# Kernel optimization log

Hardware: AMD Instinct MI355X
Metric: run time of the kernel (lower is better)

Reference implementation:

```python
import jax, jax.numpy as jnp
import numpy as np

VOCAB, D, H = 32000, 1024, 16
DH = D // H
DFF = 4 * D
EPS = 1e-5


def layer_norm(x, g, b):
    mu = jnp.mean(x, axis=-1, keepdims=True)
    var = jnp.var(x, axis=-1, keepdims=True)
    return (x - mu) * jax.lax.rsqrt(var + EPS) * g + b


def pos_enc(seq_len, d_model):
    # faithful to the torch double-loop: angle = pos / 10000**(2*i/d) for even index i
    pos = jnp.arange(seq_len, dtype=jnp.float32)[:, None]          # [S,1]
    i_even = jnp.arange(0, d_model, 2, dtype=jnp.float32)[None, :]  # [1,D/2]
    angle = pos / jnp.power(10000.0, 2.0 * i_even / d_model)        # [S,D/2]
    pe = jnp.zeros((seq_len, d_model), dtype=jnp.float32)
    pe = pe.at[:, 0::2].set(jnp.sin(angle))
    pe = pe.at[:, 1::2].set(jnp.cos(angle))
    return pe


def setup_inputs() -> dict:
    key = jax.random.key(0)
    ks = jax.random.split(key, 16)
    s = 0.02
    return {
        "tokens": jax.random.randint(ks[0], (4, 2048), 0, VOCAB),
        "emb": jax.random.normal(ks[1], (VOCAB, D), jnp.float32) * s,
        "in_proj_w": jax.random.normal(ks[2], (3 * D, D), jnp.float32) * s,
        "in_proj_b": jnp.zeros((3 * D,), jnp.float32),
        "out_proj_w": jax.random.normal(ks[3], (D, D), jnp.float32) * s,
        "out_proj_b": jnp.zeros((D,), jnp.float32),
        "w1": jax.random.normal(ks[4], (DFF, D), jnp.float32) * s,
        "b1": jnp.zeros((DFF,), jnp.float32),
        "w2": jax.random.normal(ks[5], (D, DFF), jnp.float32) * s,
        "b2": jnp.zeros((D,), jnp.float32),
        "g1": jnp.ones((D,), jnp.float32),
        "beta1": jnp.zeros((D,), jnp.float32),
        "g2": jnp.ones((D,), jnp.float32),
        "beta2": jnp.zeros((D,), jnp.float32),
    }


def reference(tokens, emb, in_proj_w, in_proj_b, out_proj_w, out_proj_b,
              w1, b1, w2, b2, g1, beta1, g2, beta2):
    B, S = tokens.shape
    x = emb[tokens] + pos_enc(S, D)[None, :, :]                 # [B,S,D]
    # multi-head self-attention (eval mode, no dropout)
    qkv = x @ in_proj_w.T + in_proj_b                           # [B,S,3D]
    q, k, v = jnp.split(qkv, 3, axis=-1)
    q = q.reshape(B, S, H, DH)
    k = k.reshape(B, S, H, DH)
    v = v.reshape(B, S, H, DH)
    scores = jnp.einsum("bqhd,bkhd->bhqk", q, k) / jnp.sqrt(jnp.float32(DH))
    attn = jax.nn.softmax(scores, axis=-1)
    ctx = jnp.einsum("bhqk,bkhd->bqhd", attn, v).reshape(B, S, D)
    attn_out = ctx @ out_proj_w.T + out_proj_b
    h = layer_norm(x + attn_out, g1, beta1)
    ff = jax.nn.relu(h @ w1.T + b1) @ w2.T + b2
    return layer_norm(h + ff, g2, beta2)
```

## Files before the change

kernel.cpp:

```cpp
#include <hip/hip_runtime.h>
#include <math.h>

#define DMODEL 1024
#define NH 16
#define DHEAD 64
#define DFF 4096
#define BATCH 4
#define SEQ 2048
#define MROWS (BATCH * SEQ)
#define LNEPS 1e-5f
#define NT (SEQ / 64)

typedef __attribute__((ext_vector_type(8))) short bf16x8;
typedef __attribute__((ext_vector_type(4))) float f32x4;
typedef __attribute__((ext_vector_type(16))) float f32x16;
typedef __attribute__((ext_vector_type(4))) unsigned int u32x4;

__device__ inline unsigned short f2bf(float f) {
  unsigned int u = __float_as_uint(f);
  unsigned int r = (u + 0x7fffu + ((u >> 16) & 1u)) >> 16;
  return (unsigned short)r;
}

__device__ inline void gload16(const unsigned short* g, char* l) {
  __builtin_amdgcn_global_load_lds(
      (const __attribute__((address_space(1))) unsigned int*)g,
      (__attribute__((address_space(3))) unsigned int*)l, 16, 0, 0);
}

__device__ inline float fexp2(float x) {
  float r;
  asm("v_exp_f32 %0, %1" : "=v"(r) : "v"(x));
  return r;
}
__device__ inline unsigned int cvtpk(float lo, float hi) {
  unsigned int r;
  asm("v_cvt_pk_bf16_f32 %0, %1, %2" : "=v"(r) : "v"(lo), "v"(hi));
  return r;
}
__device__ inline void plswap(unsigned int& a, unsigned int& b) {
  asm("v_permlane32_swap_b32 %0, %1" : "+v"(a), "+v"(b));
}

__global__ __launch_bounds__(256)
void embed_kernel(const int* __restrict__ tokens, const float* __restrict__ emb,
                  float* __restrict__ X, unsigned short* __restrict__ Xb) {
  const int HALF = DMODEL / 2;
  int idx = blockIdx.x * 256 + threadIdx.x;
  if (idx >= MROWS * HALF) return;
  int row = idx / HALF;
  int j = idx - row * HALF;
  int s = row & (SEQ - 1);
  int tok = tokens[row];
  float2 e = ((const float2*)(emb + (size_t)tok * DMODEL))[j];
  float denom = powf(10000.0f, (2.0f * (float)(2 * j)) / (float)DMODEL);
  float ang = (float)s / denom;
  float sn, cs;
  sincosf(ang, &sn, &cs);
  float2 o;
  o.x = e.x + sn;
  o.y = e.y + cs;
  ((float2*)(X + (size_t)row * DMODEL))[j] = o;
  ushort2 ob;
  ob.x = f2bf(o.x); ob.y = f2bf(o.y);
  ((ushort2*)(Xb + (size_t)row * DMODEL))[j] = ob;
}

__global__ __launch_bounds__(256)
void cvt4_kernel(const float* __restrict__ a, const float* __restrict__ b,
                 const float* __restrict__ c, const float* __restrict__ d,
                 unsigned short* __restrict__ oa, unsigned short* __restrict__ ob,
                 unsigned short* __restrict__ oc, unsigned short* __restrict__ od) {
  int i = blockIdx.x * 256 + threadIdx.x;
  const float* src; unsigned short* dst; int off;
  if (i < 786432)       { src = a; dst = oa; off = 0; }
  else if (i < 1048576) { src = b; dst = ob; off = 786432; }
  else if (i < 2097152) { src = c; dst = oc; off = 1048576; }
  else                  { src = d; dst = od; off = 2097152; }
  int j = i - off;
  float4 v = ((const float4*)src)[j];
  ushort4 o;
  o.x = f2bf(v.x); o.y = f2bf(v.y); o.z = f2bf(v.z); o.w = f2bf(v.w);
  ((ushort4*)dst)[j] = o;
}

#define AOFF(buf) ((buf) * 49152)
#define BOFF(buf) ((buf) * 49152 + 32768)

__device__ inline void stageA(const unsigned short* Ag, char* smem, int buf,
                              int m0, int K, int kt, int wv, int lane) {
  int rl = lane >> 3, c = (lane & 7) ^ rl;
#pragma unroll
  for (int i = 0; i < 4; ++i) {
    int r0 = (wv * 4 + i) * 8;
    gload16(Ag + (size_t)(m0 + r0 + rl) * K + kt * 64 + c * 8,
            smem + AOFF(buf) + r0 * 128 + lane * 16);
  }
}
__device__ inline void stageB2(const unsigned short* Bg, char* smem, int buf,
                               int n0, int K, int kt, int wv, int lane) {
  int rl = lane >> 3, c = (lane & 7) ^ rl;
#pragma unroll
  for (int i = 0; i < 2; ++i) {
    int r0 = (wv * 2 + i) * 8;
    gload16(Bg + (size_t)(n0 + r0 + rl) * K + kt * 64 + c * 8,
            smem + BOFF(buf) + r0 * 128 + lane * 16);
  }
}

#define VM6 asm volatile("s_waitcnt vmcnt(6)" ::: "memory")
#define VM0 asm volatile("s_waitcnt vmcnt(0)" ::: "memory")

#define DO_PHASE(buf, mb, LOADB, STAGE_STMT, WAIT_STMT)                         \
  {                                                                             \
    bf16x8 af[2][2];                                                            \
    _Pragma("unroll") for (int mm = 0; mm < 2; ++mm) {                          \
      int arow = wm * 64 + ((mb) + mm) * 16 + fr;                               \
      _Pragma("unroll") for (int ks = 0; ks < 2; ++ks) {                        \
        int slot = (ks * 4 + fq) ^ (arow & 7);                                  \
        af[mm][ks] = *(const bf16x8*)(smem + AOFF(buf) + arow * 128 + slot * 16); \
      }                                                                         \
    }                                                                           \
    if (LOADB) {                                                                \
      _Pragma("unroll") for (int n = 0; n < 4; ++n) {                           \
        int brow = wn * 64 + n * 16 + fr;                                       \
        _Pragma("unroll") for (int ks = 0; ks < 2; ++ks) {                      \
          int slot = (ks * 4 + fq) ^ (brow & 7);                                \
          bfr[n][ks] = *(const bf16x8*)(smem + BOFF(buf) + brow * 128 + slot * 16); \
        }                                                                       \
      }                                                                         \
    }                                                                           \
    STAGE_STMT;                                                                 \
    __builtin_amdgcn_sched_barrier(0);                                          \
    __builtin_amdgcn_s_barrier();                                               \
    __builtin_amdgcn_sched_barrier(0);                                          \
    __builtin_amdgcn_s_setprio(1);                                              \
    _Pragma("unroll") for (int mm = 0; mm < 2; ++mm)                            \
      _Pragma("unroll") for (int n = 0; n < 4; ++n)                             \
        _Pragma("unroll") for (int ks = 0; ks < 2; ++ks)                        \
          acc[(mb) + mm][n] = __builtin_amdgcn_mfma_f32_16x16x32_bf16(          \
              af[mm][ks], bfr[n][ks], acc[(mb) + mm][n], 0, 0, 0);              \
    __builtin_amdgcn_s_setprio(0);                                              \
    WAIT_STMT;                                                                  \
    __builtin_amdgcn_sched_barrier(0);                                          \
    __builtin_amdgcn_s_barrier();                                               \
    __builtin_amdgcn_sched_barrier(0);                                          \
  }

__global__ __launch_bounds__(512, 2)
void gemm8(const unsigned short* __restrict__ A, const unsigned short* __restrict__ B,
           const float* __restrict__ bias, const float* __restrict__ resid,
           float* __restrict__ Cf, unsigned short* __restrict__ Cb,
           int M, int N, int K, int relu) {
  extern __shared__ char smem[];

  const int t = threadIdx.x;
  const int lane = t & 63;
  const int wv = t >> 6;
  const int wm = wv >> 1;
  const int wn = wv & 1;
  const int fr = lane & 15;
  const int fq = lane >> 4;

  const int nwg = gridDim.x;
  const int orig = blockIdx.x;
  const int q8 = nwg >> 3;
  const int wgid = (orig & 7) * q8 + (orig >> 3);
  const int stid = wgid >> 4, within = wgid & 15;
  const int sm = within & 3, sn = within >> 2;
  const int Msup = M >> 10;
  const int stm = stid % Msup, stn = stid / Msup;
  const int m0 = (stm * 4 + sm) * 256;
  const int n0 = (stn * 4 + sn) * 128;

  f32x4 acc[4][4];
#pragma unroll
  for (int m = 0; m < 4; ++m)
#pragma unroll
    for (int n = 0; n < 4; ++n) acc[m][n] = (f32x4){0.f, 0.f, 0.f, 0.f};

  const int nk = K / 64;
  const int nj = nk / 2;

  stageB2(B, smem, 0, n0, K, 0, wv, lane);
  stageA (A, smem, 0, m0, K, 0, wv, lane);
  stageB2(B, smem, 1, n0, K, 1, wv, lane);
  stageA (A, smem, 1, m0, K, 1, wv, lane);
  VM6;
  __builtin_amdgcn_sched_barrier(0);
  __builtin_amdgcn_s_barrier();
  __builtin_amdgcn_sched_barrier(0);

  for (int j = 0; j < nj - 1; ++j) {
    const int k0 = 2 * j, k1 = 2 * j + 1;
    const int s0k = k0 + 2, s1k = k1 + 2;
    const int b0 = k0 % 3, b1 = k1 % 3;
    const int sb0 = s0k % 3, sb1 = s1k % 3;
    bf16x8 bfr[4][2];
    DO_PHASE(b0, 0, true,  stageB2(B, smem, sb0, n0, K, s0k, wv, lane), );
    DO_PHASE(b0, 2, false, stageA (A, smem, sb0, m0, K, s0k, wv, lane), VM6);
    DO_PHASE(b1, 0, true,  stageB2(B, smem, sb1, n0, K, s1k, wv, lane), );
    DO_PHASE(b1, 2, false, stageA (A, smem, sb1, m0, K, s1k, wv, lane), VM6);
  }
  {
    const int b0 = (nk - 2) % 3, b1 = (nk - 1) % 3;
    bf16x8 bfr[4][2];
    DO_PHASE(b0, 0, true,  , );
    DO_PHASE(b0, 2, false, , VM0);
    DO_PHASE(b1, 0, true,  , );
    DO_PHASE(b1, 2, false, , );
  }

  float* slab = (float*)(smem + wv * 4352);
#pragma unroll
  for (int m = 0; m < 4; ++m) {
#pragma unroll
    for (int n = 0; n < 4; ++n)
#pragma unroll
      for (int j = 0; j < 4; ++j)
        slab[(fq * 4 + j) * 68 + n * 16 + fr] = acc[m][n][j];
    int rg0 = m0 + wm * 64 + m * 16;
#pragma unroll
    for (int it = 0; it < 4; ++it) {
      int u = it * 64 + lane;
      int row = u >> 4, seg = u & 15;
      float4 v = *(const float4*)&slab[row * 68 + seg * 4];
      int col = n0 + wn * 64 + seg * 4;
      float4 b4 = *(const float4*)&bias[col];
      v.x += b4.x; v.y += b4.y; v.z += b4.z; v.w += b4.w;
      if (relu) {
        v.x = fmaxf(v.x, 0.f); v.y = fmaxf(v.y, 0.f);
        v.z = fmaxf(v.z, 0.f); v.w = fmaxf(v.w, 0.f);
      }
      size_t idx = (size_t)(rg0 + row) * N + col;
      if (resid) {
        float4 r4 = *(const float4*)&resid[idx];
        v.x += r4.x; v.y += r4.y; v.z += r4.z; v.w += r4.w;
      }
      if (Cf) {
        *(float4*)&Cf[idx] = v;
      } else {
        ushort4 ob;
        ob.x = f2bf(v.x); ob.y = f2bf(v.y); ob.z = f2bf(v.z); ob.w = f2bf(v.w);
        *(ushort4*)&Cb[idx] = ob;
      }
    }
  }
}

__global__ __launch_bounds__(512, 4)
void attn_kernel(const unsigned short* __restrict__ qkv, unsigned short* __restrict__ ctxb) {
  __shared__ __align__(16) unsigned short Ks[2][64][64];
  __shared__ __align__(16) unsigned short Vts[2][64][64];
  __shared__ __align__(16) unsigned short Slab[8][32][64];

  const int t = threadIdx.x;
  const int lane = t & 63;
  const int wq = t >> 6;
  const int l31 = lane & 31;
  const int hi1 = lane >> 5;
  const int bid = blockIdx.x;
  const int bh = bid & 63;
  const int qt = bid >> 6;
  const int b = bh >> 4, h = bh & 15;
  const int q0 = qt * 256;

  const size_t RS = 3 * DMODEL;
  const unsigned short* qb = qkv + (size_t)b * SEQ * RS + h * DHEAD;
  const unsigned short* kb = qb + DMODEL;
  const unsigned short* vb = qb + 2 * DMODEL;

  bf16x8 qf[4];
  {
    const unsigned short* qrow = qb + (size_t)(q0 + wq * 32 + l31) * RS;
#pragma unroll
    for (int s = 0; s < 4; ++s)
      qf[s] = *(const bf16x8*)(qrow + s * 16 + hi1 * 8);
  }

  const unsigned short* kgl =
      kb + (size_t)(wq * 8 + (lane >> 3)) * RS + ((lane & 7) ^ (lane >> 3)) * 8;
  const int vrow0 = wq * 8;

  f32x16 oacc[2] = {};
  float lacc = 0.f;

  gload16(kgl, (char*)&Ks[0][wq * 8][0]);
  {
    unsigned int vg[8];
#pragma unroll
    for (int e = 0; e < 8; ++e)
      vg[e] = vb[(size_t)(vrow0 + e) * RS + lane];
    uint4 u;
    u.x = vg[0] | (vg[1] << 16);
    u.y = vg[2] | (vg[3] << 16);
    u.z = vg[4] | (vg[5] << 16);
    u.w = vg[6] | (vg[7] << 16);
    *(uint4*)&Vts[0][lane][((wq ^ (lane & 7)) * 8)] = u;
  }
  __syncthreads();

  const float C = 0.18033688011112042f;

  for (int kt = 0; kt < NT; ++kt) {
    const int cur = kt & 1;
    const bool more = (kt + 1 < NT);
    unsigned int vg[8];
    if (more) {
      size_t off = (size_t)(kt + 1) * 64 * RS;
      gload16(kgl + off, (char*)&Ks[cur ^ 1][wq * 8][0]);
#pragma unroll
      for (int e = 0; e < 8; ++e)
        vg[e] = vb[off + (size_t)(vrow0 + e) * RS + lane];
    }

    f32x16 sacc[2] = {};
    __builtin_amdgcn_s_setprio(1);
#pragma unroll
    for (int s = 0; s < 4; ++s) {
#pragma unroll
      for (int kvt = 0; kvt < 2; ++kvt) {
        int row = kvt * 32 + l31;
        bf16x8 kf = *(const bf16x8*)&Ks[cur][row][(((2 * s + hi1) ^ (row & 7)) * 8)];
        sacc[kvt] = __builtin_amdgcn_mfma_f32_32x32x16_bf16(kf, qf[s], sacc[kvt], 0, 0, 0);
      }
    }
    __builtin_amdgcn_s_setprio(0);

#pragma unroll
    for (int kvt = 0; kvt < 2; ++kvt) {
      float p[16];
#pragma unroll
      for (int r = 0; r < 16; ++r) p[r] = fexp2(sacc[kvt][r] * C);
      float ps = 0.f;
#pragma unroll
      for (int r = 0; r < 16; ++r) ps += p[r];
      lacc += ps;
#pragma unroll
      for (int half = 0; half < 2; ++half) {
        const int lo = half * 8;
        unsigned int x0 = cvtpk(p[lo + 0], p[lo + 1]);
        unsigned int x1 = cvtpk(p[lo + 2], p[lo + 3]);
        unsigned int y0 = cvtpk(p[lo + 4], p[lo + 5]);
        unsigned int y1 = cvtpk(p[lo + 6], p[lo + 7]);
        plswap(x0, y0);
        plswap(x1, y1);
        bf16x8 pa = __builtin_bit_cast(bf16x8, (u32x4){x0, x1, y0, y1});
        const int s2 = kvt * 2 + half;
        __builtin_amdgcn_s_setprio(1);
#pragma unroll
        for (int dt = 0; dt < 2; ++dt) {
          int vrow = dt * 32 + l31;
          bf16x8 vf = *(const bf16x8*)&Vts[cur][vrow][(((2 * s2 + hi1) ^ (vrow & 7)) * 8)];
          oacc[dt] = __builtin_amdgcn_mfma_f32_32x32x16_bf16(pa, vf, oacc[dt], 0, 0, 0);
        }
        __builtin_amdgcn_s_setprio(0);
      }
    }

    if (more) {
      uint4 u;
      u.x = vg[0] | (vg[1] << 16);
      u.y = vg[2] | (vg[3] << 16);
      u.z = vg[4] | (vg[5] << 16);
      u.w = vg[6] | (vg[7] << 16);
      *(uint4*)&Vts[cur ^ 1][lane][((wq ^ (lane & 7)) * 8)] = u;
    }
    __syncthreads();
  }

  lacc += __shfl_xor(lacc, 32);
  float inv = 1.0f / lacc;

  float iv[16];
#pragma unroll
  for (int r = 0; r < 16; ++r)
    iv[r] = __shfl(inv, (r & 3) + 8 * (r >> 2) + 4 * hi1);

#pragma unroll
  for (int dt = 0; dt < 2; ++dt) {
    const int chunk = dt * 4 + (l31 >> 3);
    const int e7 = l31 & 7;
#pragma unroll
    for (int r = 0; r < 16; ++r) {
      int qp = (r & 3) + 8 * (r >> 2) + 4 * hi1;
      Slab[wq][qp][((chunk ^ (qp & 7)) * 8) + e7] = f2bf(oacc[dt][r] * iv[r]);
    }
  }
#pragma unroll
  for (int it = 0; it < 4; ++it) {
    int u = it * 64 + lane;
    int row = u >> 3, s = u & 7;
    uint4 v = *(const uint4*)&Slab[wq][row][((s ^ (row & 7)) * 8)];
    *(uint4*)(ctxb + (size_t)(b * SEQ + q0 + wq * 32 + row) * DMODEL + h * DHEAD + s * 8) = v;
  }
}

__global__ __launch_bounds__(256)
void ln_kernel(const float* __restrict__ Z, const float* __restrict__ g,
               const float* __restrict__ bta, float* __restrict__ Y,
               unsigned short* __restrict__ Yb) {
  const int row = blockIdx.x;
  const float4* z4 = (const float4*)(Z + (size_t)row * DMODEL);
  float4 v = z4[threadIdx.x];
  float s = v.x + v.y + v.z + v.w;
  float ss = fmaf(v.x, v.x, fmaf(v.y, v.y, fmaf(v.z, v.z, v.w * v.w)));
#pragma unroll
  for (int o = 32; o >= 1; o >>= 1) {
    s += __shfl_xor(s, o);
    ss += __shfl_xor(ss, o);
  }
  __shared__ float red[8];
  int w = threadIdx.x >> 6;
  if ((threadIdx.x & 63) == 0) { red[w] = s; red[4 + w] = ss; }
  __syncthreads();
  s = red[0] + red[1] + red[2] + red[3];
  ss = red[4] + red[5] + red[6] + red[7];
  float mu = s * (1.0f / DMODEL);
  float var = ss * (1.0f / DMODEL) - mu * mu;
  float rs = rsqrtf(var + LNEPS);
  float4 gg = ((const float4*)g)[threadIdx.x];
  float4 bb = ((const float4*)bta)[threadIdx.x];
  float4 o;
  o.x = (v.x - mu) * rs * gg.x + bb.x;
  o.y = (v.y - mu) * rs * gg.y + bb.y;
  o.z = (v.z - mu) * rs * gg.z + bb.z;
  o.w = (v.w - mu) * rs * gg.w + bb.w;
  ((float4*)(Y + (size_t)row * DMODEL))[threadIdx.x] = o;
  if (Yb) {
    ushort4 ob;
    ob.x = f2bf(o.x); ob.y = f2bf(o.y); ob.z = f2bf(o.z); ob.w = f2bf(o.w);
    ((ushort4*)(Yb + (size_t)row * DMODEL))[threadIdx.x] = ob;
  }
}

extern "C" void kernel_launch(void* const* d_in, const int* in_sizes, int n_in,
                              void* d_out, int out_size, void* d_ws, size_t ws_size,
                              hipStream_t stream) {
  const int* tokens       = (const int*)d_in[0];
  const float* emb        = (const float*)d_in[1];
  const float* in_proj_w  = (const float*)d_in[2];
  const float* in_proj_b  = (const float*)d_in[3];
  const float* out_proj_w = (const float*)d_in[4];
  const float* out_proj_b = (const float*)d_in[5];
  const float* w1         = (const float*)d_in[6];
  const float* b1         = (const float*)d_in[7];
  const float* w2         = (const float*)d_in[8];
  const float* b2         = (const float*)d_in[9];
  const float* g1         = (const float*)d_in[10];
  const float* beta1      = (const float*)d_in[11];
  const float* g2         = (const float*)d_in[12];
  const float* beta2      = (const float*)d_in[13];
  float* out = (float*)d_out;

  char* ws = (char*)d_ws;
  const size_t MB = 1ull << 20;
  unsigned short* inwb  = (unsigned short*)(ws + 0 * MB);
  unsigned short* outwb = (unsigned short*)(ws + 6 * MB);
  unsigned short* w1b   = (unsigned short*)(ws + 8 * MB);
  unsigned short* w2b   = (unsigned short*)(ws + 16 * MB);
  float* x              = (float*)(ws + 24 * MB);
  unsigned short* xb    = (unsigned short*)(ws + 56 * MB);
  unsigned short* qkvb  = (unsigned short*)(ws + 72 * MB);
  unsigned short* ctxb  = (unsigned short*)(ws + 56 * MB);
  float* h              = (float*)(ws + 72 * MB);
  unsigned short* hb    = (unsigned short*)(ws + 104 * MB);
  unsigned short* ffbb  = (unsigned short*)(ws + 120 * MB);
  float* y2             = (float*)(ws + 24 * MB);

  const size_t GLDS = 147456;

  embed_kernel<<<(MROWS * (DMODEL / 2) + 255) / 256, 256, 0, stream>>>(tokens, emb, x, xb);
  cvt4_kernel<<<12288, 256, 0, stream>>>(in_proj_w, out_proj_w, w1, w2,
                                         inwb, outwb, w1b, w2b);
  gemm8<<<(MROWS / 256) * (3 * DMODEL / 128), 512, GLDS, stream>>>(
      xb, inwb, in_proj_b, nullptr, nullptr, qkvb, MROWS, 3 * DMODEL, DMODEL, 0);
  attn_kernel<<<(SEQ / 256) * (BATCH * NH), 512, 0, stream>>>(qkvb, ctxb);
  gemm8<<<(MROWS / 256) * (DMODEL / 128), 512, GLDS, stream>>>(
      ctxb, outwb, out_proj_b, x, h, nullptr, MROWS, DMODEL, DMODEL, 0);
  ln_kernel<<<MROWS, 256, 0, stream>>>(h, g1, beta1, h, hb);
  gemm8<<<(MROWS / 256) * (DFF / 128), 512, GLDS, stream>>>(
      hb, w1b, b1, nullptr, nullptr, ffbb, MROWS, DFF, DMODEL, 1);
  gemm8<<<(MROWS / 256) * (DMODEL / 128), 512, GLDS, stream>>>(
      ffbb, w2b, b2, h, y2, nullptr, MROWS, DMODEL, DFF, 0);
  ln_kernel<<<MROWS, 256, 0, stream>>>(y2, g2, beta2, out, nullptr);
}
```

Before: 411.8 us.

## Add 256x256-tile GEMM for QKV and FFN1; pre-transpose V for attention

Adds a new gemm256 kernel that uses 256x256 output tiles with double-buffered LDS and a grouped (supertile) block order, and uses it for the QKV projection and the first FFN GEMM. Larger tiles raise arithmetic intensity and cut redundant global loads. Separately, a vtrans_kernel writes V in transposed layout to the workspace, so the attention kernel can stage V with async 16-byte loads instead of scalar gathers plus an LDS repack. The cost is an extra kernel launch and extra memory traffic for the transpose. The large tiles also lower occupancy and give fewer workgroups, which can leave some CUs underused.

```diff
diff --git a/kernel.cpp b/kernel.cpp
--- a/kernel.cpp
+++ b/kernel.cpp
@@ -84,27 +84,155 @@
   ((ushort4*)dst)[j] = o;
 }
 
+__device__ inline void stage256(const unsigned short* G, char* base, int row0,
+                                int K, int kt, int t) {
+#pragma unroll
+  for (int i = 0; i < 4; ++i) {
+    int g = i * 512 + t;
+    int row = g >> 3, sl = g & 7;
+    int c = sl ^ (row & 7);
+    gload16(G + (size_t)(row0 + row) * K + kt * 64 + c * 8, base + g * 16);
+  }
+}
+
+__global__ __launch_bounds__(512, 2)
+void gemm256(const unsigned short* __restrict__ A, const unsigned short* __restrict__ B,
+             const float* __restrict__ bias, const float* __restrict__ resid,
+             float* __restrict__ Cf, unsigned short* __restrict__ Cb,
+             int M, int N, int K, int relu) {
+  extern __shared__ char smem[];
+
+  const int t = threadIdx.x;
+  const int lane = t & 63;
+  const int wv = t >> 6;
+  const int wm = wv >> 2;
+  const int wn = wv & 3;
+  const int fr = lane & 15;
+  const int fq = lane >> 4;
+
+  const int nwg = gridDim.x;
+  const int orig = blockIdx.x;
+  const int q8 = nwg >> 3;
+  const int wgid = (orig & 7) * q8 + (orig >> 3);
+  const int stid = wgid >> 2, within = wgid & 3;
+  const int sm = within & 1, sn = within >> 1;
+  const int Msup = M >> 9;
+  const int stm = stid % Msup, stn = stid / Msup;
+  const int m0 = (stm * 2 + sm) * 256;
+  const int n0 = (stn * 2 + sn) * 256;
+
+  f32x4 acc[8][4];
+#pragma unroll
+  for (int m = 0; m < 8; ++m)
+#pragma unroll
+    for (int n = 0; n < 4; ++n) acc[m][n] = (f32x4){0.f, 0.f, 0.f, 0.f};
+
+  const int nk = K / 64;
+
+  stage256(A, smem, m0, K, 0, t);
+  stage256(B, smem + 32768, n0, K, 0, t);
+
+  for (int kt = 0; kt < nk; ++kt) {
+    const int buf = kt & 1;
+    asm volatile("s_waitcnt vmcnt(0)" ::: "memory");
+    __builtin_amdgcn_s_barrier();
+    if (kt + 1 < nk) {
+      char* nxt = smem + ((buf ^ 1) << 16);
+      stage256(A, nxt, m0, K, kt + 1, t);
+      stage256(B, nxt + 32768, n0, K, kt + 1, t);
+    }
+    const unsigned short* Al = (const unsigned short*)(smem + (buf << 16));
+    const unsigned short* Bl = (const unsigned short*)(smem + (buf << 16) + 32768);
+
+    bf16x8 bfr[4][2];
+#pragma unroll
+    for (int n = 0; n < 4; ++n) {
+      int brow = wn * 64 + n * 16 + fr;
+#pragma unroll
+      for (int ks = 0; ks < 2; ++ks)
+        bfr[n][ks] = *(const bf16x8*)&Bl[brow * 64 + (((ks * 4 + fq) ^ (brow & 7)) * 8)];
+    }
+#pragma unroll
+    for (int mp = 0; mp < 4; ++mp) {
+      bf16x8 af[2][2];
+#pragma unroll
+      for (int mm = 0; mm < 2; ++mm) {
+        int arow = wm * 128 + (mp * 2 + mm) * 16 + fr;
+#pragma unroll
+        for (int ks = 0; ks < 2; ++ks)
+          af[mm][ks] = *(const bf16x8*)&Al[arow * 64 + (((ks * 4 + fq) ^ (arow & 7)) * 8)];
+      }
+      __builtin_amdgcn_s_setprio(1);
+#pragma unroll
+      for (int mm = 0; mm < 2; ++mm)
+#pragma unroll
+        for (int n = 0; n < 4; ++n)
+#pragma unroll
+          for (int ks = 0; ks < 2; ++ks)
+            acc[mp * 2 + mm][n] = __builtin_amdgcn_mfma_f32_16x16x32_bf16(
+                af[mm][ks], bfr[n][ks], acc[mp * 2 + mm][n], 0, 0, 0);
+      __builtin_amdgcn_s_setprio(0);
+    }
+  }
+
+  float* slab = (float*)(smem + wv * 4352);
+#pragma unroll
+  for (int m = 0; m < 8; ++m) {
+#pragma unroll
+    for (int n = 0; n < 4; ++n)
+#pragma unroll
+      for (int j = 0; j < 4; ++j)
+        slab[(fq * 4 + j) * 68 + n * 16 + fr] = acc[m][n][j];
+    int rg0 = m0 + wm * 128 + m * 16;
+#pragma unroll
+    for (int it = 0; it < 4; ++it) {
+      int u = it * 64 + lane;
+      int row = u >> 4, seg = u & 15;
+      float4 v = *(const float4*)&slab[row * 68 + seg * 4];
+      int col = n0 + wn * 64 + seg * 4;
+      float4 b4 = *(const float4*)&bias[col];
+      v.x += b4.x; v.y += b4.y; v.z += b4.z; v.w += b4.w;
+      if (relu) {
+        v.x = fmaxf(v.x, 0.f); v.y = fmaxf(v.y, 0.f);
+        v.z = fmaxf(v.z, 0.f); v.w = fmaxf(v.w, 0.f);
+      }
+      size_t idx = (size_t)(rg0 + row) * N + col;
+      if (resid) {
+        float4 r4 = *(const float4*)&resid[idx];
+        v.x += r4.x; v.y += r4.y; v.z += r4.z; v.w += r4.w;
+      }
+      if (Cf) {
+        *(float4*)&Cf[idx] = v;
+      } else {
+        ushort4 ob;
+        ob.x = f2bf(v.x); ob.y = f2bf(v.y); ob.z = f2bf(v.z); ob.w = f2bf(v.w);
+        *(ushort4*)&Cb[idx] = ob;
+      }
+    }
+  }
+}
+
 #define AOFF(buf) ((buf) * 49152)
 #define BOFF(buf) ((buf) * 49152 + 32768)
 
-__device__ inline void stageA(const unsigned short* Ag, char* smem, int buf,
+__device__ inline void stageA(const unsigned short* Ag, char* smem_, int buf,
                               int m0, int K, int kt, int wv, int lane) {
   int rl = lane >> 3, c = (lane & 7) ^ rl;
 #pragma unroll
   for (int i = 0; i < 4; ++i) {
     int r0 = (wv * 4 + i) * 8;
     gload16(Ag + (size_t)(m0 + r0 + rl) * K + kt * 64 + c * 8,
-            smem + AOFF(buf) + r0 * 128 + lane * 16);
-  }
-}
-__device__ inline void stageB2(const unsigned short* Bg, char* smem, int buf,
+            smem_ + AOFF(buf) + r0 * 128 + lane * 16);
+  }
+}
+__device__ inline void stageB2(const unsigned short* Bg, char* smem_, int buf,
                                int n0, int K, int kt, int wv, int lane) {
   int rl = lane >> 3, c = (lane & 7) ^ rl;
 #pragma unroll
   for (int i = 0; i < 2; ++i) {
     int r0 = (wv * 2 + i) * 8;
     gload16(Bg + (size_t)(n0 + r0 + rl) * K + kt * 64 + c * 8,
-            smem + BOFF(buf) + r0 * 128 + lane * 16);
+            smem_ + BOFF(buf) + r0 * 128 + lane * 16);
   }
 }
 
@@ -248,8 +376,44 @@
   }
 }
 
+__global__ __launch_bounds__(256)
+void vtrans_kernel(const unsigned short* __restrict__ qkvb, unsigned short* __restrict__ vtb) {
+  __shared__ __align__(16) unsigned short tile[64][64];
+  const int st = blockIdx.x;
+  const int bh = blockIdx.y;
+  const int b = bh >> 4, h = bh & 15;
+  const int t = threadIdx.x;
+#pragma unroll
+  for (int p = 0; p < 2; ++p) {
+    int item = p * 256 + t;
+    int r = item >> 3, c8 = item & 7;
+    const unsigned short* src =
+        qkvb + (size_t)(b * SEQ + st * 64 + r) * (3 * DMODEL) + 2048 + h * 64 + c8 * 8;
+    *(uint4*)&tile[r][(c8 ^ (r & 7)) * 8] = *(const uint4*)src;
+  }
+  __syncthreads();
+#pragma unroll
+  for (int p = 0; p < 2; ++p) {
+    int item = p * 256 + t;
+    int d = item & 63, s8 = item >> 6;
+    unsigned short v[8];
+#pragma unroll
+    for (int e = 0; e < 8; ++e) {
+      int s = s8 * 8 + e;
+      v[e] = tile[s][(((d >> 3) ^ (s & 7)) * 8) + (d & 7)];
+    }
+    uint4 u;
+    u.x = (unsigned int)v[0] | ((unsigned int)v[1] << 16);
+    u.y = (unsigned int)v[2] | ((unsigned int)v[3] << 16);
+    u.z = (unsigned int)v[4] | ((unsigned int)v[5] << 16);
+    u.w = (unsigned int)v[6] | ((unsigned int)v[7] << 16);
+    *(uint4*)(vtb + ((size_t)bh * 64 + d) * SEQ + st * 64 + s8 * 8) = u;
+  }
+}
+
 __global__ __launch_bounds__(512, 4)
-void attn_kernel(const unsigned short* __restrict__ qkv, unsigned short* __restrict__ ctxb) {
+void attn_kernel(const unsigned short* __restrict__ qkv, const unsigned short* __restrict__ vtb,
+                 unsigned short* __restrict__ ctxb) {
   __shared__ __align__(16) unsigned short Ks[2][64][64];
   __shared__ __align__(16) unsigned short Vts[2][64][64];
   __shared__ __align__(16) unsigned short Slab[8][32][64];
@@ -268,7 +432,6 @@
   const size_t RS = 3 * DMODEL;
   const unsigned short* qb = qkv + (size_t)b * SEQ * RS + h * DHEAD;
   const unsigned short* kb = qb + DMODEL;
-  const unsigned short* vb = qb + 2 * DMODEL;
 
   bf16x8 qf[4];
   {
@@ -280,38 +443,23 @@
 
   const unsigned short* kgl =
       kb + (size_t)(wq * 8 + (lane >> 3)) * RS + ((lane & 7) ^ (lane >> 3)) * 8;
-  const int vrow0 = wq * 8;
+  const unsigned short* vgl =
+      vtb + ((size_t)bh * 64 + wq * 8 + (lane >> 3)) * SEQ + ((lane & 7) ^ (lane >> 3)) * 8;
 
   f32x16 oacc[2] = {};
   float lacc = 0.f;
 
   gload16(kgl, (char*)&Ks[0][wq * 8][0]);
-  {
-    unsigned int vg[8];
-#pragma unroll
-    for (int e = 0; e < 8; ++e)
-      vg[e] = vb[(size_t)(vrow0 + e) * RS + lane];
-    uint4 u;
-    u.x = vg[0] | (vg[1] << 16);
-    u.y = vg[2] | (vg[3] << 16);
-    u.z = vg[4] | (vg[5] << 16);
-    u.w = vg[6] | (vg[7] << 16);
-    *(uint4*)&Vts[0][lane][((wq ^ (lane & 7)) * 8)] = u;
-  }
+  gload16(vgl, (char*)&Vts[0][wq * 8][0]);
   __syncthreads();
 
   const float C = 0.18033688011112042f;
 
   for (int kt = 0; kt < NT; ++kt) {
     const int cur = kt & 1;
-    const bool more = (kt + 1 < NT);
-    unsigned int vg[8];
-    if (more) {
-      size_t off = (size_t)(kt + 1) * 64 * RS;
-      gload16(kgl + off, (char*)&Ks[cur ^ 1][wq * 8][0]);
-#pragma unroll
-      for (int e = 0; e < 8; ++e)
-        vg[e] = vb[off + (size_t)(vrow0 + e) * RS + lane];
+    if (kt + 1 < NT) {
+      gload16(kgl + (size_t)(kt + 1) * 64 * RS, (char*)&Ks[cur ^ 1][wq * 8][0]);
+      gload16(vgl + (size_t)(kt + 1) * 64, (char*)&Vts[cur ^ 1][wq * 8][0]);
     }
 
     f32x16 sacc[2] = {};
@@ -356,15 +504,6 @@
         }
         __builtin_amdgcn_s_setprio(0);
       }
-    }
-
-    if (more) {
-      uint4 u;
-      u.x = vg[0] | (vg[1] << 16);
-      u.y = vg[2] | (vg[3] << 16);
-      u.z = vg[4] | (vg[5] << 16);
-      u.w = vg[6] | (vg[7] << 16);
-      *(uint4*)&Vts[cur ^ 1][lane][((wq ^ (lane & 7)) * 8)] = u;
     }
     __syncthreads();
   }
@@ -462,26 +601,29 @@
   float* x              = (float*)(ws + 24 * MB);
   unsigned short* xb    = (unsigned short*)(ws + 56 * MB);
   unsigned short* qkvb  = (unsigned short*)(ws + 72 * MB);
+  unsigned short* vtb   = (unsigned short*)(ws + 120 * MB);
   unsigned short* ctxb  = (unsigned short*)(ws + 56 * MB);
   float* h              = (float*)(ws + 72 * MB);
   unsigned short* hb    = (unsigned short*)(ws + 104 * MB);
   unsigned short* ffbb  = (unsigned short*)(ws + 120 * MB);
   float* y2             = (float*)(ws + 24 * MB);
 
-  const size_t GLDS = 147456;
+  const size_t GLDS8 = 147456;
+  const size_t GLDS256 = 131072;
 
   embed_kernel<<<(MROWS * (DMODEL / 2) + 255) / 256, 256, 0, stream>>>(tokens, emb, x, xb);
   cvt4_kernel<<<12288, 256, 0, stream>>>(in_proj_w, out_proj_w, w1, w2,
                                          inwb, outwb, w1b, w2b);
-  gemm8<<<(MROWS / 256) * (3 * DMODEL / 128), 512, GLDS, stream>>>(
+  gemm256<<<(MROWS / 256) * (3 * DMODEL / 256), 512, GLDS256, stream>>>(
       xb, inwb, in_proj_b, nullptr, nullptr, qkvb, MROWS, 3 * DMODEL, DMODEL, 0);
-  attn_kernel<<<(SEQ / 256) * (BATCH * NH), 512, 0, stream>>>(qkvb, ctxb);
-  gemm8<<<(MROWS / 256) * (DMODEL / 128), 512, GLDS, stream>>>(
+  vtrans_kernel<<<dim3(SEQ / 64, BATCH * NH), 256, 0, stream>>>(qkvb, vtb);
+  attn_kernel<<<(SEQ / 256) * (BATCH * NH), 512, 0, stream>>>(qkvb, vtb, ctxb);
+  gemm8<<<(MROWS / 256) * (DMODEL / 128), 512, GLDS8, stream>>>(
       ctxb, outwb, out_proj_b, x, h, nullptr, MROWS, DMODEL, DMODEL, 0);
   ln_kernel<<<MROWS, 256, 0, stream>>>(h, g1, beta1, h, hb);
-  gemm8<<<(MROWS / 256) * (DFF / 128), 512, GLDS, stream>>>(
+  gemm256<<<(MROWS / 256) * (DFF / 256), 512, GLDS256, stream>>>(
       hb, w1b, b1, nullptr, nullptr, ffbb, MROWS, DFF, DMODEL, 1);
-  gemm8<<<(MROWS / 256) * (DMODEL / 128), 512, GLDS, stream>>>(
+  gemm8<<<(MROWS / 256) * (DMODEL / 128), 512, GLDS8, stream>>>(
       ffbb, w2b, b2, h, y2, nullptr, MROWS, DMODEL, DFF, 0);
   ln_kernel<<<MROWS, 256, 0, stream>>>(y2, g2, beta2, out, nullptr);
 }
```

Result: no change. 413.6 us (+0.4%).
